# Optimization experiments

Hardware: AMD Instinct MI355X
Metric: run time of the kernel (lower is better)

## Reference

```python
import jax, jax.numpy as jnp
import numpy as np
import math

B, S, D_EMB = 1, 4096, 768
N_HEADS, D_QKV = 12, 64
INV_TEMP = 1.0


def setup_inputs() -> dict:
    key = jax.random.key(0)
    ks = jax.random.split(key, 11)
    s = 0.02
    return {
        "q_in": jax.random.normal(ks[0], (B, S, D_EMB), jnp.float32),
        "k_in": jax.random.normal(ks[1], (B, S, D_EMB), jnp.float32),
        "v_in": jax.random.normal(ks[2], (B, S, D_EMB), jnp.float32),
        "W_q": jax.random.normal(ks[3], (D_EMB, N_HEADS * D_QKV), jnp.float32) * s,
        "b_q": jnp.zeros((N_HEADS * D_QKV,), jnp.float32),
        "W_k": jax.random.normal(ks[4], (D_EMB, N_HEADS * D_QKV), jnp.float32) * s,
        "b_k": jnp.zeros((N_HEADS * D_QKV,), jnp.float32),
        "W_v": jax.random.normal(ks[5], (D_EMB, N_HEADS * D_QKV), jnp.float32) * s,
        "b_v": jnp.zeros((N_HEADS * D_QKV,), jnp.float32),
        "W_o": jax.random.normal(ks[6], (N_HEADS * D_QKV, D_EMB), jnp.float32) * s,
        "b_o": jnp.zeros((D_EMB,), jnp.float32),
    }


def _split_heads(x):  # [B,S,H*D] -> [B,H,S,D]
    b, s, _ = x.shape
    return x.reshape(b, s, N_HEADS, D_QKV).transpose(0, 2, 1, 3)


def reference(q_in, k_in, v_in, W_q, b_q, W_k, b_k, W_v, b_v, W_o, b_o):
    q = _split_heads(q_in @ W_q + b_q)
    k = _split_heads(k_in @ W_k + b_k)
    v = _split_heads(v_in @ W_v + b_v)
    # full [B,H,S,S] score matrix (module materializes it for custom masking)
    scores = INV_TEMP * jnp.einsum('bhqd,bhkd->bhqk', q, k) / math.sqrt(D_QKV)
    attn = jax.nn.softmax(scores, axis=-1)
    out = jnp.einsum('bhqk,bhkd->bhqd', attn, v)  # [B,H,S,D]
    out = out.transpose(0, 2, 1, 3).reshape(q_in.shape[0], q_in.shape[1], N_HEADS * D_QKV)
    return out @ W_o + b_o
```

## Files before the change

kernel.cpp:

```cpp
#include <hip/hip_runtime.h>

#define S 4096
#define E 768
#define NH 12
#define DH 64
#define QSCALE (0.125f * 1.44269504f)
#define KSPLIT 4

typedef __bf16 bf16;
typedef __bf16 bf16x4 __attribute__((ext_vector_type(4)));
typedef __bf16 bf16x8 __attribute__((ext_vector_type(8)));
typedef float  f32x4  __attribute__((ext_vector_type(4)));

#define MFMA(a, b, c) __builtin_amdgcn_mfma_f32_16x16x32_bf16(a, b, c, 0, 0, 0)

__device__ __forceinline__ void async16(const bf16* g, bf16* l) {
  __builtin_amdgcn_global_load_lds(
      (const __attribute__((address_space(1))) void*)g,
      (__attribute__((address_space(3))) void*)l, 16, 0, 0);
}

__global__ __launch_bounds__(256) void prologue(const float* __restrict__ q_in,
                                                const float* __restrict__ k_in,
                                                const float* __restrict__ v_in,
                                                const float* __restrict__ w0,
                                                const float* __restrict__ w1,
                                                const float* __restrict__ w2,
                                                const float* __restrict__ w3,
                                                bf16* __restrict__ qb,
                                                bf16* __restrict__ kb,
                                                bf16* __restrict__ vb,
                                                bf16* __restrict__ t0,
                                                bf16* __restrict__ t1,
                                                bf16* __restrict__ t2,
                                                bf16* __restrict__ t3) {
  const int bid = blockIdx.x, tid = threadIdx.x;
  if (bid < 2304) {
    const int z = bid / 576, rem = bid % 576;
    const int bx = rem % 24, by = rem / 24;
    const float* W = z == 0 ? w0 : (z == 1 ? w1 : (z == 2 ? w2 : w3));
    bf16* Wt = z == 0 ? t0 : (z == 1 ? t1 : (z == 2 ? t2 : t3));
    __shared__ float t[32][33];
    const int tx = tid & 31, ty = tid >> 5;
    for (int j = ty; j < 32; j += 8)
      t[j][tx] = W[(by * 32 + j) * E + bx * 32 + tx];
    __syncthreads();
    for (int j = ty; j < 32; j += 8)
      Wt[(bx * 32 + j) * E + by * 32 + tx] = (bf16)t[tx][j];
  } else {
    const int b2 = bid - 2304;
    const int z = b2 / 3072, r2 = b2 % 3072;
    const float* in = z == 0 ? q_in : (z == 1 ? k_in : v_in);
    bf16* out = z == 0 ? qb : (z == 1 ? kb : vb);
    const int i = r2 * 1024 + tid * 4;
    float4 v = *(const float4*)(in + i);
    bf16x4 o = { (bf16)v.x, (bf16)v.y, (bf16)v.z, (bf16)v.w };
    *(bf16x4*)(out + i) = o;
  }
}

__global__ __launch_bounds__(256) void gemm128(const bf16* __restrict__ A0,
                                               const bf16* __restrict__ A1,
                                               const bf16* __restrict__ A2,
                                               const bf16* __restrict__ B0,
                                               const bf16* __restrict__ B1,
                                               const bf16* __restrict__ B2,
                                               const float* __restrict__ bias0,
                                               const float* __restrict__ bias1,
                                               const float* __restrict__ bias2,
                                               bf16* __restrict__ C0,
                                               bf16* __restrict__ C1,
                                               bf16* __restrict__ C2) {
  __shared__ __align__(16) bf16 smem[128 * 136];
  bf16* Asm = smem;
  bf16* Bsm = smem + 4096;
  bf16* Cs  = smem;

  const int z = blockIdx.z;
  const bf16* A  = z == 0 ? A0 : (z == 1 ? A1 : A2);
  const bf16* Bt = z == 0 ? B0 : (z == 1 ? B1 : B2);
  const float* bias = z == 0 ? bias0 : (z == 1 ? bias1 : bias2);

  const int tid = threadIdx.x;
  const int wv = tid >> 6, lane = tid & 63;
  const int quad = lane >> 4, l16 = lane & 15;
  const int m0 = blockIdx.x * 128, n0 = blockIdx.y * 128;
  const int wm = (wv >> 1) * 64, wn = (wv & 1) * 64;
  const int srow = lane >> 2, scol = (lane & 3) * 8;

  f32x4 acc[4][4] = {};

  for (int k0 = 0; k0 < E; k0 += 32) {
#pragma unroll
    for (int j = 0; j < 2; j++) {
      const int ch = wv * 2 + j;
      async16(&A[(size_t)(m0 + ch * 16 + srow) * E + k0 + scol], &Asm[ch * 512]);
      async16(&Bt[(size_t)(n0 + ch * 16 + srow) * E + k0 + scol], &Bsm[ch * 512]);
    }
    __syncthreads();
    bf16x8 af[4], bfv[4];
#pragma unroll
    for (int mi = 0; mi < 4; mi++)
      af[mi] = *(const bf16x8*)&Asm[(wm + mi * 16 + l16) * 32 + quad * 8];
#pragma unroll
    for (int ni = 0; ni < 4; ni++)
      bfv[ni] = *(const bf16x8*)&Bsm[(wn + ni * 16 + l16) * 32 + quad * 8];
#pragma unroll
    for (int mi = 0; mi < 4; mi++)
#pragma unroll
      for (int ni = 0; ni < 4; ni++)
        acc[mi][ni] = MFMA(af[mi], bfv[ni], acc[mi][ni]);
    __syncthreads();
  }

  const float scale = (z == 0) ? QSCALE : 1.0f;
#pragma unroll
  for (int mi = 0; mi < 4; mi++) {
#pragma unroll
    for (int ni = 0; ni < 4; ni++) {
      const int nl = wn + ni * 16 + l16;
      const float bv = bias[n0 + nl];
#pragma unroll
      for (int r = 0; r < 4; r++) {
        const int ml = wm + mi * 16 + quad * 4 + r;
        const float v = (acc[mi][ni][r] + bv) * scale;
        if (z == 2) Cs[nl * 136 + ml] = (bf16)v;
        else        Cs[ml * 136 + nl] = (bf16)v;
      }
    }
  }
  __syncthreads();

  if (z == 0) {
    const int e = lane & 7;
#pragma unroll
    for (int p = 0; p < 8; p++) {
      const int hr = p * 32 + wv * 8 + (lane >> 3);
      const int r = hr >> 1, hf = hr & 1;
      bf16x8 c = *(const bf16x8*)&Cs[r * 136 + hf * 64 + e * 8];
      *(bf16x8*)(C0 + (size_t)((n0 >> 6) + hf) * S * DH + (size_t)(m0 + r) * DH + e * 8) = c;
    }
  } else {
    bf16* dst = (z == 1) ? C1 : C2;
#pragma unroll
    for (int p = 0; p < 8; p++) {
      const int cid = p * 4 + wv;
      const int reg = cid >> 3;
      const int i = cid & 7;
      const int h_l = reg >> 1, tile = reg & 1;
      bf16x8 c;
      if (z == 1) {
        const int row = tile * 64 + (i >> 1) * 16 + l16;
        const int col = h_l * 64 + (i & 1) * 32 + quad * 8;
        c = *(const bf16x8*)&Cs[row * 136 + col];
      } else {
        const int nl = h_l * 64 + (i >> 1) * 16 + l16;
        const int ml = tile * 64 + (i & 1) * 32 + quad * 8;
        c = *(const bf16x8*)&Cs[nl * 136 + ml];
      }
      *(bf16x8*)(dst + (size_t)((n0 >> 6) + h_l) * S * DH +
                 (size_t)((m0 >> 6) + tile) * 4096 + i * 512 + lane * 8) = c;
    }
  }
}

__global__ __launch_bounds__(256, 3) void attn(const bf16* __restrict__ Q,
                                               const bf16* __restrict__ Kf,
                                               const bf16* __restrict__ Vf,
                                               bf16* __restrict__ Op0,
                                               bf16* __restrict__ Op1,
                                               bf16* __restrict__ Op2,
                                               bf16* __restrict__ Op3,
                                               float* __restrict__ Lp) {
  __shared__ __align__(16) bf16 P2[4][64][72];
  const int flat = blockIdx.x + 16 * (blockIdx.y + 12 * blockIdx.z);
  const int swz = (flat & 7) * 96 + (flat >> 3);
  const int qt = swz & 15;
  const int rem = swz >> 4;
  const int ks = rem & 3;
  const int h = rem >> 2;

  const int tid = threadIdx.x;
  const int wave = tid >> 6, lane = tid & 63;
  const int quad = lane >> 4, l16 = lane & 15;
  const int q0 = qt * 256 + wave * 64;

  const bf16* Qh = Q + (size_t)h * S * DH;
  const bf16* kbase = Kf + (size_t)h * S * DH + (size_t)ks * (S / KSPLIT) * DH + lane * 8;
  const bf16* vbase = Vf + (size_t)h * S * DH + (size_t)ks * (S / KSPLIT) * DH + lane * 8;
  bf16* Op = ks == 0 ? Op0 : (ks == 1 ? Op1 : (ks == 2 ? Op2 : Op3));

  bf16x8 aq[4][2];
#pragma unroll
  for (int qb = 0; qb < 4; qb++)
#pragma unroll
    for (int j = 0; j < 2; j++)
      aq[qb][j] = *(const bf16x8*)&Qh[(size_t)(q0 + qb * 16 + l16) * DH + j * 32 + quad * 8];

  bf16x8 ones;
#pragma unroll
  for (int e = 0; e < 8; e++) ones[e] = (bf16)1.0f;

  f32x4 o[4][4] = {};
  f32x4 ol[4] = {};

  bf16* Pw = &P2[wave][0][0];

  const int T = (S / KSPLIT) / 64;
  for (int t = 0; t < T; ++t) {
    const bf16* kp = kbase + (size_t)t * 4096;
    bf16x8 kr[8];
#pragma unroll
    for (int i = 0; i < 8; i++) kr[i] = *(const bf16x8*)(kp + i * 512);

#pragma unroll
    for (int kb = 0; kb < 4; kb++)
#pragma unroll
      for (int qb = 0; qb < 4; qb++) {
        f32x4 st = {};
        st = MFMA(kr[kb * 2], aq[qb][0], st);
        st = MFMA(kr[kb * 2 + 1], aq[qb][1], st);
        bf16x4 pk;
#pragma unroll
        for (int r = 0; r < 4; r++) pk[r] = (bf16)__builtin_exp2f(st[r]);
        *(bf16x4*)&Pw[(qb * 16 + l16) * 72 + kb * 16 + quad * 4] = pk;
      }

    bf16x8 bp[4][2];
#pragma unroll
    for (int qb = 0; qb < 4; qb++)
#pragma unroll
      for (int jc = 0; jc < 2; jc++)
        bp[qb][jc] = *(const bf16x8*)&Pw[(qb * 16 + l16) * 72 + jc * 32 + quad * 8];

#pragma unroll
    for (int qb = 0; qb < 4; qb++) {
      ol[qb] = MFMA(ones, bp[qb][0], ol[qb]);
      ol[qb] = MFMA(ones, bp[qb][1], ol[qb]);
    }

    const bf16* vp = vbase + (size_t)t * 4096;
#pragma unroll
    for (int db = 0; db < 4; db++) {
      bf16x8 v0 = *(const bf16x8*)(vp + (db * 2) * 512);
      bf16x8 v1 = *(const bf16x8*)(vp + (db * 2 + 1) * 512);
#pragma unroll
      for (int qb = 0; qb < 4; qb++) {
        o[db][qb] = MFMA(v0, bp[qb][0], o[db][qb]);
        o[db][qb] = MFMA(v1, bp[qb][1], o[db][qb]);
      }
    }
  }

  float* Lph = Lp + (size_t)(ks * NH + h) * S;
  if (quad == 0) {
#pragma unroll
    for (int qb = 0; qb < 4; qb++)
      Lph[q0 + qb * 16 + l16] = ol[qb][0];
  }
#pragma unroll
  for (int db = 0; db < 4; db++)
#pragma unroll
    for (int qb = 0; qb < 4; qb++) {
      bf16x4 pk;
#pragma unroll
      for (int r = 0; r < 4; r++) pk[r] = (bf16)o[db][qb][r];
      *(bf16x4*)&Pw[(qb * 16 + l16) * 72 + db * 16 + quad * 4] = pk;
    }
  {
    const int rr = lane >> 3, ee = (lane & 7) * 8;
#pragma unroll
    for (int p = 0; p < 8; p++) {
      const int row = p * 8 + rr;
      bf16x8 c = *(const bf16x8*)&Pw[row * 72 + ee];
      *(bf16x8*)(Op + (size_t)(q0 + row) * E + h * DH + ee) = c;
    }
  }
}

__global__ __launch_bounds__(256) void combine(const bf16* __restrict__ Op0,
                                               const bf16* __restrict__ Op1,
                                               const bf16* __restrict__ Op2,
                                               const bf16* __restrict__ Op3,
                                               const float* __restrict__ Lp,
                                               bf16* __restrict__ Obf) {
  const int i8 = blockIdx.x * 256 + threadIdx.x;
  const size_t base = (size_t)i8 * 8;
  const int row = (int)(base / E), c = (int)(base % E);
  const int h = c >> 6;
  const float l = Lp[(size_t)h * S + row] + Lp[(size_t)(NH + h) * S + row] +
                  Lp[(size_t)(2 * NH + h) * S + row] + Lp[(size_t)(3 * NH + h) * S + row];
  const float rl = 1.0f / l;
  bf16x8 a = *(const bf16x8*)(Op0 + base);
  bf16x8 b = *(const bf16x8*)(Op1 + base);
  bf16x8 cc = *(const bf16x8*)(Op2 + base);
  bf16x8 d = *(const bf16x8*)(Op3 + base);
  bf16x8 o;
#pragma unroll
  for (int e = 0; e < 8; e++)
    o[e] = (bf16)((((float)a[e] + (float)b[e]) + ((float)cc[e] + (float)d[e])) * rl);
  *(bf16x8*)(Obf + base) = o;
}

__global__ __launch_bounds__(256) void gemm64(const bf16* __restrict__ A,
                                              const bf16* __restrict__ Bt,
                                              const float* __restrict__ bias,
                                              float* __restrict__ C) {
  __shared__ __align__(16) bf16 Asm[2][64 * 32];
  __shared__ __align__(16) bf16 Bsm[2][64 * 32];
  const int tid = threadIdx.x;
  const int wv = tid >> 6, lane = tid & 63;
  const int quad = lane >> 4, l16 = lane & 15;
  const int m0 = blockIdx.x * 64, n0 = blockIdx.y * 64;
  const int srow = lane >> 2, scol = (lane & 3) * 8;

  f32x4 acc[4] = {};

  for (int k0 = 0; k0 < E; k0 += 64) {
#pragma unroll
    for (int jc = 0; jc < 2; jc++) {
      async16(&A[(size_t)(m0 + wv * 16 + srow) * E + k0 + jc * 32 + scol], &Asm[jc][wv * 512]);
      async16(&Bt[(size_t)(n0 + wv * 16 + srow) * E + k0 + jc * 32 + scol], &Bsm[jc][wv * 512]);
    }
    __syncthreads();
#pragma unroll
    for (int jc = 0; jc < 2; jc++) {
      bf16x8 af = *(const bf16x8*)&Asm[jc][(wv * 16 + l16) * 32 + quad * 8];
#pragma unroll
      for (int ni = 0; ni < 4; ni++) {
        bf16x8 bfr = *(const bf16x8*)&Bsm[jc][(ni * 16 + l16) * 32 + quad * 8];
        acc[ni] = MFMA(af, bfr, acc[ni]);
      }
    }
    __syncthreads();
  }

  const int row0 = m0 + wv * 16 + quad * 4;
#pragma unroll
  for (int ni = 0; ni < 4; ni++) {
    const int col = n0 + ni * 16 + l16;
    const float bv = bias[col];
#pragma unroll
    for (int r = 0; r < 4; r++)
      C[(size_t)(row0 + r) * E + col] = acc[ni][r] + bv;
  }
}

extern "C" void kernel_launch(void* const* d_in, const int* in_sizes, int n_in,
                              void* d_out, int out_size, void* d_ws, size_t ws_size,
                              hipStream_t stream) {
  (void)in_sizes; (void)n_in; (void)out_size; (void)ws_size;
  const float* q_in = (const float*)d_in[0];
  const float* k_in = (const float*)d_in[1];
  const float* v_in = (const float*)d_in[2];
  const float* W_q  = (const float*)d_in[3];
  const float* b_q  = (const float*)d_in[4];
  const float* W_k  = (const float*)d_in[5];
  const float* b_k  = (const float*)d_in[6];
  const float* W_v  = (const float*)d_in[7];
  const float* b_v  = (const float*)d_in[8];
  const float* W_o  = (const float*)d_in[9];
  const float* b_o  = (const float*)d_in[10];

  const size_t SE2 = (size_t)S * E * 2;
  const size_t EE2 = (size_t)E * E * 2;
  char* ws = (char*)d_ws;
  bf16* qb  = (bf16*)(ws);
  bf16* kb  = (bf16*)(ws + SE2);
  bf16* vb  = (bf16*)(ws + 2 * SE2);
  bf16* WqT = (bf16*)(ws + 3 * SE2);
  bf16* WkT = (bf16*)(ws + 3 * SE2 + EE2);
  bf16* WvT = (bf16*)(ws + 3 * SE2 + 2 * EE2);
  bf16* WoT = (bf16*)(ws + 3 * SE2 + 3 * EE2);
  bf16* Qh  = (bf16*)(ws + 3 * SE2 + 4 * EE2);
  bf16* Kf  = (bf16*)(ws + 4 * SE2 + 4 * EE2);
  bf16* Vf  = (bf16*)(ws + 5 * SE2 + 4 * EE2);
  bf16* Obf = (bf16*)(ws + 6 * SE2 + 4 * EE2);
  bf16* Op1 = qb;
  bf16* Op2 = kb;
  bf16* Op3 = vb;
  float* Lp = (float*)WqT;

  prologue<<<dim3(2304 + 3 * 3072), 256, 0, stream>>>(
      q_in, k_in, v_in, W_q, W_k, W_v, W_o, qb, kb, vb, WqT, WkT, WvT, WoT);

  gemm128<<<dim3(S / 128, E / 128, 3), 256, 0, stream>>>(
      qb, kb, vb, WqT, WkT, WvT, b_q, b_k, b_v, Qh, Kf, Vf);

  attn<<<dim3(S / 256, NH, KSPLIT), 256, 0, stream>>>(Qh, Kf, Vf, Obf, Op1, Op2, Op3, Lp);

  combine<<<dim3(S * E / 2048), 256, 0, stream>>>(Obf, Op1, Op2, Op3, Lp, Obf);

  gemm64<<<dim3(S / 64, E / 64), 256, 0, stream>>>(Obf, WoT, b_o, (float*)d_out);
}
```

Baseline: 226.5 us.

## Fuse split-K partial combine into output projection GEMM A-tile load

Removes the separate combine kernel and instead sums the four split-K attention partials and applies the 1/l normalization while loading A tiles in the output GEMM. Per-row reciprocal sums are precomputed into shared memory per block. This eliminates one launch and the write/read of the combined bf16 buffer, but each GEMM block now reads four partial buffers and the A load becomes synchronous register loads instead of async LDS loads, multiplying redundant reads across column blocks.

```diff
diff --git a/kernel.cpp b/kernel.cpp
--- a/kernel.cpp
+++ b/kernel.cpp
@@ -278,49 +278,54 @@
   }
 }
 
-__global__ __launch_bounds__(256) void combine(const bf16* __restrict__ Op0,
+__global__ __launch_bounds__(256) void gemm64c(const bf16* __restrict__ Op0,
                                                const bf16* __restrict__ Op1,
                                                const bf16* __restrict__ Op2,
                                                const bf16* __restrict__ Op3,
                                                const float* __restrict__ Lp,
-                                               bf16* __restrict__ Obf) {
-  const int i8 = blockIdx.x * 256 + threadIdx.x;
-  const size_t base = (size_t)i8 * 8;
-  const int row = (int)(base / E), c = (int)(base % E);
-  const int h = c >> 6;
-  const float l = Lp[(size_t)h * S + row] + Lp[(size_t)(NH + h) * S + row] +
-                  Lp[(size_t)(2 * NH + h) * S + row] + Lp[(size_t)(3 * NH + h) * S + row];
-  const float rl = 1.0f / l;
-  bf16x8 a = *(const bf16x8*)(Op0 + base);
-  bf16x8 b = *(const bf16x8*)(Op1 + base);
-  bf16x8 cc = *(const bf16x8*)(Op2 + base);
-  bf16x8 d = *(const bf16x8*)(Op3 + base);
-  bf16x8 o;
-#pragma unroll
-  for (int e = 0; e < 8; e++)
-    o[e] = (bf16)((((float)a[e] + (float)b[e]) + ((float)cc[e] + (float)d[e])) * rl);
-  *(bf16x8*)(Obf + base) = o;
-}
-
-__global__ __launch_bounds__(256) void gemm64(const bf16* __restrict__ A,
-                                              const bf16* __restrict__ Bt,
-                                              const float* __restrict__ bias,
-                                              float* __restrict__ C) {
+                                               const bf16* __restrict__ Bt,
+                                               const float* __restrict__ bias,
+                                               float* __restrict__ C) {
   __shared__ __align__(16) bf16 Asm[2][64 * 32];
   __shared__ __align__(16) bf16 Bsm[2][64 * 32];
+  __shared__ float Linv[NH * 64];
   const int tid = threadIdx.x;
   const int wv = tid >> 6, lane = tid & 63;
   const int quad = lane >> 4, l16 = lane & 15;
   const int m0 = blockIdx.x * 64, n0 = blockIdx.y * 64;
   const int srow = lane >> 2, scol = (lane & 3) * 8;
 
+#pragma unroll
+  for (int it = 0; it < 3; ++it) {
+    const int idx = tid + it * 256;
+    const int hh = idx >> 6, r = idx & 63;
+    const int row = m0 + r;
+    const float l = Lp[(size_t)hh * S + row] + Lp[(size_t)(NH + hh) * S + row] +
+                    Lp[(size_t)(2 * NH + hh) * S + row] + Lp[(size_t)(3 * NH + hh) * S + row];
+    Linv[idx] = 1.0f / l;
+  }
+  __syncthreads();
+
   f32x4 acc[4] = {};
 
   for (int k0 = 0; k0 < E; k0 += 64) {
+    const int hh = k0 >> 6;
+#pragma unroll
+    for (int jc = 0; jc < 2; jc++)
+      async16(&Bt[(size_t)(n0 + wv * 16 + srow) * E + k0 + jc * 32 + scol], &Bsm[jc][wv * 512]);
+    const float rl = Linv[hh * 64 + wv * 16 + srow];
 #pragma unroll
     for (int jc = 0; jc < 2; jc++) {
-      async16(&A[(size_t)(m0 + wv * 16 + srow) * E + k0 + jc * 32 + scol], &Asm[jc][wv * 512]);
-      async16(&Bt[(size_t)(n0 + wv * 16 + srow) * E + k0 + jc * 32 + scol], &Bsm[jc][wv * 512]);
+      const size_t ai = (size_t)(m0 + wv * 16 + srow) * E + k0 + jc * 32 + scol;
+      bf16x8 a0 = *(const bf16x8*)(Op0 + ai);
+      bf16x8 a1 = *(const bf16x8*)(Op1 + ai);
+      bf16x8 a2 = *(const bf16x8*)(Op2 + ai);
+      bf16x8 a3 = *(const bf16x8*)(Op3 + ai);
+      bf16x8 cmb;
+#pragma unroll
+      for (int e = 0; e < 8; e++)
+        cmb[e] = (bf16)((((float)a0[e] + (float)a1[e]) + ((float)a2[e] + (float)a3[e])) * rl);
+      *(bf16x8*)&Asm[jc][wv * 512 + lane * 8] = cmb;
     }
     __syncthreads();
 #pragma unroll
@@ -375,7 +380,7 @@
   bf16* Qh  = (bf16*)(ws + 3 * SE2 + 4 * EE2);
   bf16* Kf  = (bf16*)(ws + 4 * SE2 + 4 * EE2);
   bf16* Vf  = (bf16*)(ws + 5 * SE2 + 4 * EE2);
-  bf16* Obf = (bf16*)(ws + 6 * SE2 + 4 * EE2);
+  bf16* Op0 = (bf16*)(ws + 6 * SE2 + 4 * EE2);
   bf16* Op1 = qb;
   bf16* Op2 = kb;
   bf16* Op3 = vb;
@@ -387,9 +392,8 @@
   gemm128<<<dim3(S / 128, E / 128, 3), 256, 0, stream>>>(
       qb, kb, vb, WqT, WkT, WvT, b_q, b_k, b_v, Qh, Kf, Vf);
 
-  attn<<<dim3(S / 256, NH, KSPLIT), 256, 0, stream>>>(Qh, Kf, Vf, Obf, Op1, Op2, Op3, Lp);
-
-  combine<<<dim3(S * E / 2048), 256, 0, stream>>>(Obf, Op1, Op2, Op3, Lp, Obf);
-
-  gemm64<<<dim3(S / 64, E / 64), 256, 0, stream>>>(Obf, WoT, b_o, (float*)d_out);
-}
+  attn<<<dim3(S / 256, NH, KSPLIT), 256, 0, stream>>>(Qh, Kf, Vf, Op0, Op1, Op2, Op3, Lp);
+
+  gemm64c<<<dim3(S / 64, E / 64), 256, 0, stream>>>(
+      Op0, Op1, Op2, Op3, Lp, WoT, b_o, (float*)d_out);
+}
```

Measured after the change: 234.7 us. 3.6% more time.
